# Optimization experiments

Measured on AMD Instinct MI355X. Metric: run time of the kernel, lower is better.

The kernel has to match this reference:

```python
import jax, jax.numpy as jnp
import numpy as np

SEG_NUMS = [1, 2, 4, 8, 16, 32, 64, 128, 256, 512]
L = SEG_NUMS[-1]
B, C, VOCAB = 32, 64, 8192
BETA = 0.25
RESI = 0.5  # quant_resi_ratio
N_PHI = 4
# PhiPartiallyShared ticks for K==4: linspace(1/(3K), 1-1/(3K), K)
PHI_TICKS = np.linspace(1.0 / (3 * N_PHI), 1.0 - 1.0 / (3 * N_PHI), N_PHI)


def interp_area(x, size):
    """torch F.interpolate(mode='area') for [B,C,l] when sizes divide evenly."""
    b, c, l = x.shape
    if size == l:
        return x
    if size < l:  # adaptive avg pool == block mean (l % size == 0)
        return x.reshape(b, c, size, l // size).mean(axis=-1)
    return jnp.repeat(x, size // l, axis=-1)  # area upsample == repeat


def phi_apply(h, w, b):
    """Phi: h*(1-r) + Conv1d(h)*r, same padding, ks=3. h:[B,C,l] w:[C,C,3] b:[C]."""
    y = jax.lax.conv_general_dilated(h, w, window_strides=(1,), padding=[(1, 1)],
                                     dimension_numbers=('NCH', 'OIH', 'NCH'))
    y = y + b[None, :, None]
    return h * (1.0 - RESI) + y * RESI


def _normalize(x, axis):
    return x / jnp.maximum(jnp.linalg.norm(x, axis=axis, keepdims=True), 1e-12)


def _mse(a, b):
    return jnp.mean((a - b) ** 2)


def setup_inputs() -> dict:
    key = jax.random.key(0)
    k1, k2, k3 = jax.random.split(key, 3)
    f_BCl = jax.random.normal(k1, (B, C, L), jnp.float32)
    embed_w = jax.random.normal(k2, (VOCAB, C), jnp.float32)
    phi_w = jax.random.normal(k3, (N_PHI, C, C, 3), jnp.float32) * 0.05  # conv-init scale
    phi_b = jnp.zeros((N_PHI, C), jnp.float32)
    return {"f_BCl": f_BCl, "embed_w": embed_w, "phi_w": phi_w, "phi_b": phi_b}


def vq_forward(f, embed_w, phi_w, phi_b):
    f = f.astype(jnp.float32)
    f_ng = jax.lax.stop_gradient(f)
    f_rest = f_ng
    f_hat = jnp.zeros_like(f_ng)
    loss = jnp.asarray(0.0, jnp.float32)
    # argmax uses .data (stop-grad) normalized codebook columns
    cb_n = _normalize(jax.lax.stop_gradient(embed_w), axis=1)  # [V, C]
    num_scales = len(SEG_NUMS)
    for si, s in enumerate(SEG_NUMS):
        rest = interp_area(f_rest, s)                      # [B, C, s] (identity at last scale)
        rest_NC = _normalize(rest.transpose(0, 2, 1).reshape(-1, C), axis=1)  # [B*s, C]
        idx = jnp.argmax(rest_NC @ cb_n.T, axis=1)         # [B*s] cosine-sim lookup
        h = embed_w[idx].reshape(B, s, C).transpose(0, 2, 1)  # gather (differentiable) -> [B,C,s]
        h = interp_area(h, L)
        pidx = int(np.argmin(np.abs(PHI_TICKS - si / (num_scales - 1))))
        h = phi_apply(h, phi_w[pidx], phi_b[pidx])
        f_hat = f_hat + h
        f_rest = f_rest - h
        loss = loss + BETA * _mse(jax.lax.stop_gradient(f_hat), f) + _mse(f_hat, f_ng)
    loss = loss / num_scales
    f_hat_out = jax.lax.stop_gradient(f_hat) - f_ng + f  # straight-through
    return f_hat_out, loss


def reference(f_BCl, embed_w, phi_w, phi_b):
    return vq_forward(f_BCl, embed_w, phi_w, phi_b)
```

## Files before the change

kernel.cpp:

```cpp
#include <hip/hip_runtime.h>


#define B_ 32
#define C_ 64
#define L_ 512
#define V_ 8192

typedef _Float16 half8 __attribute__((ext_vector_type(8)));
typedef float f32x4 __attribute__((ext_vector_type(4)));

#define C11 4.8828125e-4f

__device__ __forceinline__ unsigned enc_f(float s) {
  unsigned u = __float_as_uint(s);
  return (u & 0x80000000u) ? ~u : (u | 0x80000000u);
}

__device__ __forceinline__ void split2(float x, _Float16& h, _Float16& m) {
  h = (_Float16)x;
  float r1 = x - (float)h;
  m = (_Float16)(r1 * 2048.0f);
}

__global__ __launch_bounds__(256) void k_setup(
    const float* __restrict__ f, const float* __restrict__ embed,
    const float* __restrict__ phiw, _Float16* __restrict__ ch,
    _Float16* __restrict__ cm, float* __restrict__ restAll,
    float* __restrict__ lossac, unsigned long long* __restrict__ packed,
    float* __restrict__ phiwT) {
  const int blk = blockIdx.x;
  const int tid = threadIdx.x;
  if (blk < 128) {
    int g = blk * 256 + tid;
    int v = g >> 2;
    int sub = g & 3;
    const float* row = embed + v * 64 + sub * 16;
    float x[16];
    float ss = 0.f;
#pragma unroll
    for (int i = 0; i < 16; i += 4) {
      float4 t = *(const float4*)(row + i);
      x[i] = t.x; x[i + 1] = t.y; x[i + 2] = t.z; x[i + 3] = t.w;
      ss += t.x * t.x + t.y * t.y + t.z * t.z + t.w * t.w;
    }
    ss += __shfl_xor(ss, 1);
    ss += __shfl_xor(ss, 2);
    float rinv = 1.0f / fmaxf(sqrtf(ss), 1e-12f);
    _Float16 hb[16], mb[16];
#pragma unroll
    for (int i = 0; i < 16; i++) split2(x[i] * rinv, hb[i], mb[i]);
    const int o = v * 64 + sub * 16;
    *(half8*)(ch + o) = *(half8*)(hb);
    *(half8*)(ch + o + 8) = *(half8*)(hb + 8);
    *(half8*)(cm + o) = *(half8*)(mb);
    *(half8*)(cm + o + 8) = *(half8*)(mb + 8);
  } else if (blk < 640) {
    int sb = blk - 128;
    int b = sb >> 4;
    int c = (sb & 15) * 4 + (tid >> 6);
    int lane = tid & 63;
    const float* row = f + (b * 64 + c) * 512 + lane * 8;
    float4 x0 = *(const float4*)row;
    float4 x1 = *(const float4*)(row + 4);
    float ssum = ((x0.x + x0.y) + (x0.z + x0.w)) +
                 ((x1.x + x1.y) + (x1.z + x1.w));
#pragma unroll
    for (int off = 32; off > 0; off >>= 1) ssum += __shfl_down(ssum, off);
    if (lane == 0) restAll[c * 32 + b] = ssum;
  } else {
    int zg = (blk - 640) * 256 + tid;
    const int ZS = 512 * 256;
    for (int i = zg; i < 126976; i += ZS) restAll[2048 + i] = 0.0f;
    for (int i = zg; i < 32736; i += ZS) packed[i] = 0ull;
    if (zg < 16) lossac[zg] = 0.0f;
    if (phiwT) {
      for (int i = zg; i < 49152; i += ZS) {
        float v = phiw[i];
        int p = i / 12288;
        int r = i - p * 12288;
        int o = r / 192;
        int r2 = r - o * 192;
        int c = r2 / 3;
        int t = r2 - c * 3;
        phiwT[((p * 3 + t) * 64 + c) * 64 + o] = v;
      }
    }
  }
}

#define ARG_LOAD(BH0, BH1, BM0, BM1, TT)                                   \
  {                                                                        \
    const _Float16* p1 = ch + (code_start + (TT) + m) * 64 + quad * 8;     \
    const _Float16* p2 = cm + (code_start + (TT) + m) * 64 + quad * 8;     \
    BH0 = *(const half8*)(p1);                                             \
    BH1 = *(const half8*)(p1 + 32);                                        \
    BM0 = *(const half8*)(p2);                                             \
    BM1 = *(const half8*)(p2 + 32);                                        \
  }

#define ARG_TILE(BH0, BH1, BM0, BM1, TT)                                   \
  {                                                                        \
    const int cid = cs_g + (TT) + m;                                       \
    _Pragma("unroll") for (int mt = 0; mt < MT; mt++) {                    \
      f32x4 a0, a1;                                                        \
      a0 = __builtin_amdgcn_mfma_f32_16x16x32_f16(ah[mt][0], BH0, Z, 0, 0, 0); \
      a1 = __builtin_amdgcn_mfma_f32_16x16x32_f16(ah[mt][0], BM0, Z, 0, 0, 0); \
      a1 = __builtin_amdgcn_mfma_f32_16x16x32_f16(am[mt][0], BH0, a1, 0, 0, 0); \
      a0 = __builtin_amdgcn_mfma_f32_16x16x32_f16(ah[mt][1], BH1, a0, 0, 0, 0); \
      a1 = __builtin_amdgcn_mfma_f32_16x16x32_f16(ah[mt][1], BM1, a1, 0, 0, 0); \
      a1 = __builtin_amdgcn_mfma_f32_16x16x32_f16(am[mt][1], BH1, a1, 0, 0, 0); \
      _Pragma("unroll") for (int r = 0; r < 4; r++) {                      \
        float sc = fmaf(C11, a1[r], a0[r]);                                \
        if (sc > best[mt][r]) { best[mt][r] = sc; bidx[mt][r] = cid; }     \
      }                                                                    \
    }                                                                      \
  }

template <int MT>
__global__ __launch_bounds__(256, 2) void k_argmax3(
    const _Float16* __restrict__ ch, const _Float16* __restrict__ cm,
    const float* __restrict__ restq, unsigned long long* __restrict__ packedq,
    int Q, int mgroups, int wave_codes, int cbase) {
  const int mg = blockIdx.x % mgroups;
  const int sp = blockIdx.x / mgroups;
  const int lane = threadIdx.x & 63;
  const int wave = threadIdx.x >> 6;
  const int qbase = mg * (MT * 16);
  __shared__ _Float16 qh[MT * 16][72];
  __shared__ _Float16 qm[MT * 16][72];
  __shared__ unsigned long long spart[4][MT * 16];
  for (int i = threadIdx.x; i < MT * 16 * 64; i += 256) {
    int c = i / (MT * 16);
    int qq = i % (MT * 16);
    float v = restq[c * Q + qbase + qq];
    _Float16 h, m;
    split2(v, h, m);
    qh[qq][c] = h;
    qm[qq][c] = m;
  }
  __syncthreads();

  const int m = lane & 15;
  const int quad = lane >> 4;
  half8 ah[MT][2], am[MT][2];
#pragma unroll
  for (int mt = 0; mt < MT; mt++)
#pragma unroll
    for (int kc = 0; kc < 2; kc++) {
      ah[mt][kc] = *(const half8*)(&qh[mt * 16 + m][kc * 32 + quad * 8]);
      am[mt][kc] = *(const half8*)(&qm[mt * 16 + m][kc * 32 + quad * 8]);
    }

  float best[MT][4];
  int bidx[MT][4];
#pragma unroll
  for (int mt = 0; mt < MT; mt++)
#pragma unroll
    for (int r = 0; r < 4; r++) { best[mt][r] = -3.4e38f; bidx[mt][r] = 0; }

  const int code_start = (sp * 4 + wave) * wave_codes;
  const int cs_g = cbase + code_start;
  const f32x4 Z = {0.f, 0.f, 0.f, 0.f};

  half8 Ah0, Ah1, Am0, Am1, Bh0, Bh1, Bm0, Bm1;
  ARG_LOAD(Ah0, Ah1, Am0, Am1, 0);
  if (16 < wave_codes) ARG_LOAD(Bh0, Bh1, Bm0, Bm1, 16);
  for (int t = 0; t < wave_codes; t += 32) {
    ARG_TILE(Ah0, Ah1, Am0, Am1, t);
    if (t + 32 < wave_codes) ARG_LOAD(Ah0, Ah1, Am0, Am1, t + 32);
    if (t + 16 < wave_codes) {
      ARG_TILE(Bh0, Bh1, Bm0, Bm1, t + 16);
      if (t + 48 < wave_codes) ARG_LOAD(Bh0, Bh1, Bm0, Bm1, t + 48);
    }
  }

#pragma unroll
  for (int off = 1; off < 16; off <<= 1) {
#pragma unroll
    for (int mt = 0; mt < MT; mt++)
#pragma unroll
      for (int r = 0; r < 4; r++) {
        float ob = __shfl_xor(best[mt][r], off);
        int oi = __shfl_xor(bidx[mt][r], off);
        if (ob > best[mt][r] || (ob == best[mt][r] && oi < bidx[mt][r])) {
          best[mt][r] = ob; bidx[mt][r] = oi;
        }
      }
  }
  if (m == 0) {
#pragma unroll
    for (int mt = 0; mt < MT; mt++)
#pragma unroll
      for (int r = 0; r < 4; r++) {
        unsigned long long pk =
            ((unsigned long long)enc_f(best[mt][r]) << 32) |
            (unsigned)(~bidx[mt][r]);
        spart[wave][mt * 16 + quad * 4 + r] = pk;
      }
  }
  __syncthreads();
  if (threadIdx.x < MT * 16) {
    unsigned long long v = spart[0][threadIdx.x];
    unsigned long long v1 = spart[1][threadIdx.x];
    unsigned long long v2 = spart[2][threadIdx.x];
    unsigned long long v3 = spart[3][threadIdx.x];
    if (v1 > v) v = v1;
    if (v2 > v) v = v2;
    if (v3 > v) v = v3;
    atomicMax(&packedq[qbase + threadIdx.x], v);
  }
}

__global__ __launch_bounds__(256) void k_fused(
    const float* __restrict__ f, const float* __restrict__ embed,
    const float* __restrict__ phiw, const float* __restrict__ phib,
    const float* __restrict__ wT, const unsigned long long* __restrict__ packedq,
    float* __restrict__ restn, float* __restrict__ fhat,
    float* __restrict__ lossac, int s, int log2blk, int pidx, int si,
    int log2blkn) {
  const int ch0 = blockIdx.x * 32;
  const int bb = blockIdx.y;
  const int tid = threadIdx.x;
  const int blkw = 1 << log2blk;
  int j_lo = (ch0 >> log2blk) - 1;
  if (j_lo < 0) j_lo = 0;
  int j_hi = ((ch0 + 31) >> log2blk) + 1;
  if (j_hi > s - 1) j_hi = s - 1;
  const int nseg = j_hi - j_lo + 1;

  __shared__ float hl[34][64];
  __shared__ float abc_l[34][192];

  for (int i = tid; i < nseg * 64; i += 256) {
    int seg = i >> 6, c = i & 63;
    int idx = (int)(~(unsigned)(packedq[bb * s + j_lo + seg]));
    hl[seg][c] = embed[idx * 64 + c];
  }
  __syncthreads();

  {
    const int o = tid & 63;
    const int w4 = tid >> 6;
    const float* wrow = phiw + (pidx * 64 + o) * 192;
    const float* wtp = wT ? (wT + pidx * 12288 + o) : nullptr;
    float acc[9][3];
#pragma unroll
    for (int a = 0; a < 9; a++) { acc[a][0] = acc[a][1] = acc[a][2] = 0.f; }
#pragma unroll
    for (int c4b = 0; c4b < 4; c4b++) {
      float w48[48];
      if (wT) {
        const float* wp = wtp + c4b * 16 * 64;
#pragma unroll
        for (int cc = 0; cc < 16; cc++)
#pragma unroll
          for (int k = 0; k < 3; k++)
            w48[cc * 3 + k] = wp[(k * 64 + cc) * 64];
      } else {
#pragma unroll
        for (int k = 0; k < 12; k++)
          *(float4*)(w48 + 4 * k) = *(const float4*)(wrow + c4b * 48 + 4 * k);
      }
#pragma unroll
      for (int sx = 0; sx < 9; sx++) {
        int seg = w4 + sx * 4;
        if (seg < nseg) {
#pragma unroll
          for (int cc4 = 0; cc4 < 4; cc4++) {
            float4 h4 = *(const float4*)(&hl[seg][c4b * 16 + cc4 * 4]);
            const float hv[4] = {h4.x, h4.y, h4.z, h4.w};
#pragma unroll
            for (int u = 0; u < 4; u++) {
              int cc = cc4 * 4 + u;
              acc[sx][0] = fmaf(w48[cc * 3 + 0], hv[u], acc[sx][0]);
              acc[sx][1] = fmaf(w48[cc * 3 + 1], hv[u], acc[sx][1]);
              acc[sx][2] = fmaf(w48[cc * 3 + 2], hv[u], acc[sx][2]);
            }
          }
        }
      }
    }
#pragma unroll
    for (int sx = 0; sx < 9; sx++) {
      int seg = w4 + sx * 4;
      if (seg < nseg) {
        abc_l[seg][o] = acc[sx][0];
        abc_l[seg][64 + o] = acc[sx][1];
        abc_l[seg][128 + o] = acc[sx][2];
      }
    }
  }
  __syncthreads();

  const int c = tid >> 2;
  const int l0 = ch0 + (tid & 3) * 8;
  const float bias = phib[pidx * 64 + c];
  const int fi0 = (bb * 64 + c) * 512 + l0;
  const float4 fa = *(const float4*)(f + fi0);
  const float4 fb2 = *(const float4*)(f + fi0 + 4);
  float fv[8] = {fa.x, fa.y, fa.z, fa.w, fb2.x, fb2.y, fb2.z, fb2.w};
  float fhv[8] = {0.f, 0.f, 0.f, 0.f, 0.f, 0.f, 0.f, 0.f};
  if (si != 0) {
    const float4 ga = *(const float4*)(fhat + fi0);
    const float4 gb2 = *(const float4*)(fhat + fi0 + 4);
    fhv[0] = ga.x; fhv[1] = ga.y; fhv[2] = ga.z; fhv[3] = ga.w;
    fhv[4] = gb2.x; fhv[5] = gb2.y; fhv[6] = gb2.z; fhv[7] = gb2.w;
  }
  float dv[8];
  float sq = 0.f;
#pragma unroll
  for (int k = 0; k < 8; k++) {
    int l = l0 + k;
    int j = l >> log2blk;
    int jrel = j - j_lo;
    int pos = l & (blkw - 1);
    float y = abc_l[jrel][64 + c] + bias;
    if (pos == 0) {
      if (j > 0) y += abc_l[jrel - 1][c];
    } else {
      y += abc_l[jrel][c];
    }
    if (pos == blkw - 1) {
      if (j < s - 1) y += abc_l[jrel + 1][128 + c];
    } else {
      y += abc_l[jrel][128 + c];
    }
    float ho = 0.5f * (hl[jrel][c] + y);
    float fh = fhv[k] + ho;
    fhv[k] = fh;
    float d = fh - fv[k];
    dv[k] = d;
    sq = fmaf(d, d, sq);
  }
  *(float4*)(fhat + fi0) = make_float4(fhv[0], fhv[1], fhv[2], fhv[3]);
  *(float4*)(fhat + fi0 + 4) = make_float4(fhv[4], fhv[5], fhv[6], fhv[7]);

  if (log2blkn >= 0) {
    const int sn = 512 >> log2blkn;
    const int blkn = 1 << log2blkn;
    const int qb = c * (32 * sn) + bb * sn;
    if (blkn >= 16) {
      float rs = -(((dv[0] + dv[1]) + (dv[2] + dv[3])) +
                   ((dv[4] + dv[5]) + (dv[6] + dv[7])));
      atomicAdd(&restn[qb + (l0 >> log2blkn)], rs);
    } else if (blkn == 8) {
      float rs = -(((dv[0] + dv[1]) + (dv[2] + dv[3])) +
                   ((dv[4] + dv[5]) + (dv[6] + dv[7])));
      restn[qb + (l0 >> 3)] = rs;
    } else {
      for (int base = 0; base < 8; base += blkn) {
        float rs = 0.f;
        for (int k = 0; k < blkn; k++) rs += dv[base + k];
        restn[qb + ((l0 + base) >> log2blkn)] = -rs;
      }
    }
  }

#pragma unroll
  for (int off = 32; off > 0; off >>= 1) sq += __shfl_down(sq, off);
  __shared__ float red[4];
  const int lane = tid & 63, wave = tid >> 6;
  if (lane == 0) red[wave] = sq;
  __syncthreads();
  if (tid == 0)
    atomicAdd(&lossac[si], (red[0] + red[1]) + (red[2] + red[3]));
}

__global__ void k_loss(const float* __restrict__ lossac,
                       float* __restrict__ out) {
  if (threadIdx.x == 0 && blockIdx.x == 0) {
    float sum = 0.f;
    for (int i = 0; i < 10; i++) sum += lossac[i];
    out[B_ * C_ * L_] = sum * (1.25f / (10.0f * (float)(B_ * C_ * L_)));
  }
}

extern "C" void kernel_launch(void* const* d_in, const int* in_sizes, int n_in,
                              void* d_out, int out_size, void* d_ws,
                              size_t ws_size, hipStream_t stream) {
  const float* f     = (const float*)d_in[0];
  const float* embed = (const float*)d_in[1];
  const float* phiw  = (const float*)d_in[2];
  const float* phib  = (const float*)d_in[3];
  float* fhat = (float*)d_out;

  _Float16* ch = (_Float16*)d_ws;
  _Float16* cm = ch + V_ * 64;
  float* restAll = (float*)(cm + V_ * 64);
  float* lossac = restAll + 2048 * 1023;
  unsigned long long* packed = (unsigned long long*)(lossac + 16);
  float* phiwT = (float*)(packed + 32736);
  const size_t WS_NEED = (size_t)((char*)(phiwT + 49152) - (char*)d_ws);
  if (ws_size < WS_NEED) phiwT = nullptr;

  static const int PIDX[10] = {0, 0, 1, 1, 1, 2, 2, 3, 3, 3};
  static const int NSPL[10] = {16, 16, 16, 16, 16, 16, 16, 16, 8, 4};

  k_setup<<<dim3(1152), dim3(256), 0, stream>>>(f, embed, phiw, ch, cm,
                                                restAll, lossac, packed,
                                                phiwT);

  for (int si = 0; si < 10; si++) {
    const int s = 1 << si;
    const int Q = 32 * s;
    const int log2blk = 9 - si;
    const int nsplit = NSPL[si];
    const float* restq = restAll + 2048 * (s - 1);
    unsigned long long* pq = packed + 32 * (s - 1);

    const int nhalves = (si == 9) ? 2 : 1;
    const int codes_per = V_ / nhalves;
    const int wave_codes = codes_per / nsplit / 4;
    for (int hf = 0; hf < nhalves; hf++) {
      const int cbase = hf * codes_per;
      const _Float16* chp = ch + (size_t)cbase * 64;
      const _Float16* cmp = cm + (size_t)cbase * 64;
      if (Q >= 64) {
        const int mgroups = Q / 64;
        k_argmax3<4><<<dim3(mgroups * nsplit), dim3(256), 0, stream>>>(
            chp, cmp, restq, pq, Q, mgroups, wave_codes, cbase);
      } else {
        k_argmax3<2><<<dim3(nsplit), dim3(256), 0, stream>>>(
            chp, cmp, restq, pq, Q, 1, wave_codes, cbase);
      }
    }

    float* restn = (si < 9) ? (restAll + 2048 * (2 * s - 1)) : nullptr;
    const int log2blkn = (si < 9) ? (8 - si) : -1;
    k_fused<<<dim3(16, 32), dim3(256), 0, stream>>>(
        f, embed, phiw, phib, phiwT, pq, restn, fhat, lossac, s, log2blk,
        PIDX[si], si, log2blkn);
  }
  k_loss<<<dim3(1), dim3(64), 0, stream>>>(lossac, fhat);
}
```

Measured before the change: 635.1 us.

## Pre-swizzle fp16 codebook into MFMA fragment layout and drop half-split launches

The setup kernel now writes the split fp16 codebook (high and residual parts) in a blocked layout of 16 codes by 32 channels. Each lane's half8 fragment sits contiguously, so a wave reads a tile with fully coalesced lane*8 loads instead of strided per-code rows. The last scale no longer splits the codebook into two halves with separate launches; one launch covers all 8192 codes. This cuts uncoalesced global traffic and launch overhead, at the cost of a fixed layout that every reader of ch/cm must agree on.

```diff
diff --git a/kernel.cpp b/kernel.cpp
--- a/kernel.cpp
+++ b/kernel.cpp
@@ -49,11 +49,15 @@
     _Float16 hb[16], mb[16];
 #pragma unroll
     for (int i = 0; i < 16; i++) split2(x[i] * rinv, hb[i], mb[i]);
-    const int o = v * 64 + sub * 16;
-    *(half8*)(ch + o) = *(half8*)(hb);
-    *(half8*)(ch + o + 8) = *(half8*)(hb + 8);
-    *(half8*)(cm + o) = *(half8*)(mb);
-    *(half8*)(cm + o + 8) = *(half8*)(mb + 8);
+    const int kc = sub >> 1;
+    const int q0 = (2 * sub) & 3;
+    const int q1 = (2 * sub + 1) & 3;
+    const int m = v & 15;
+    const int blkbase = ((v >> 4) * 2 + kc) * 512;
+    *(half8*)(ch + blkbase + (q0 * 16 + m) * 8) = *(half8*)(hb);
+    *(half8*)(ch + blkbase + (q1 * 16 + m) * 8) = *(half8*)(hb + 8);
+    *(half8*)(cm + blkbase + (q0 * 16 + m) * 8) = *(half8*)(mb);
+    *(half8*)(cm + blkbase + (q1 * 16 + m) * 8) = *(half8*)(mb + 8);
   } else if (blk < 640) {
     int sb = blk - 128;
     int b = sb >> 4;
@@ -90,12 +94,12 @@
 
 #define ARG_LOAD(BH0, BH1, BM0, BM1, TT)                                   \
   {                                                                        \
-    const _Float16* p1 = ch + (code_start + (TT) + m) * 64 + quad * 8;     \
-    const _Float16* p2 = cm + (code_start + (TT) + m) * 64 + quad * 8;     \
+    const _Float16* p1 = ch + (code_start + (TT)) * 64 + lane * 8;         \
+    const _Float16* p2 = cm + (code_start + (TT)) * 64 + lane * 8;         \
     BH0 = *(const half8*)(p1);                                             \
-    BH1 = *(const half8*)(p1 + 32);                                        \
+    BH1 = *(const half8*)(p1 + 512);                                       \
     BM0 = *(const half8*)(p2);                                             \
-    BM1 = *(const half8*)(p2 + 32);                                        \
+    BM1 = *(const half8*)(p2 + 512);                                       \
   }
 
 #define ARG_TILE(BH0, BH1, BM0, BM1, TT)                                   \
@@ -405,24 +409,17 @@
     const int Q = 32 * s;
     const int log2blk = 9 - si;
     const int nsplit = NSPL[si];
+    const int wave_codes = V_ / nsplit / 4;
     const float* restq = restAll + 2048 * (s - 1);
     unsigned long long* pq = packed + 32 * (s - 1);
 
-    const int nhalves = (si == 9) ? 2 : 1;
-    const int codes_per = V_ / nhalves;
-    const int wave_codes = codes_per / nsplit / 4;
-    for (int hf = 0; hf < nhalves; hf++) {
-      const int cbase = hf * codes_per;
-      const _Float16* chp = ch + (size_t)cbase * 64;
-      const _Float16* cmp = cm + (size_t)cbase * 64;
-      if (Q >= 64) {
-        const int mgroups = Q / 64;
-        k_argmax3<4><<<dim3(mgroups * nsplit), dim3(256), 0, stream>>>(
-            chp, cmp, restq, pq, Q, mgroups, wave_codes, cbase);
-      } else {
-        k_argmax3<2><<<dim3(nsplit), dim3(256), 0, stream>>>(
-            chp, cmp, restq, pq, Q, 1, wave_codes, cbase);
-      }
+    if (Q >= 64) {
+      const int mgroups = Q / 64;
+      k_argmax3<4><<<dim3(mgroups * nsplit), dim3(256), 0, stream>>>(
+          ch, cm, restq, pq, Q, mgroups, wave_codes, 0);
+    } else {
+      k_argmax3<2><<<dim3(nsplit), dim3(256), 0, stream>>>(
+          ch, cm, restq, pq, Q, 1, wave_codes, 0);
     }
 
     float* restn = (si < 9) ? (restAll + 2048 * (2 * s - 1)) : nullptr;
```

Result: faster. 569.3 us (-10.4%).
